# Kernel tuning notes

Hardware: AMD Instinct MI355X
Metric: run time of the kernel (lower is better)

## Reference

```python
import jax, jax.numpy as jnp
import numpy as np

B, V, DIM = 64, 64, 512
H = 2 * DIM  # 1024 hidden units


def setup_inputs() -> dict:
    key = jax.random.key(0)
    ks = jax.random.split(key, 7)
    scale = 0.05
    return {
        "state": jax.random.normal(ks[0], (B, DIM), jnp.float32),
        "action": jax.random.normal(ks[1], (B, DIM), jnp.float32),
        "embed": jax.random.normal(ks[2], (V, DIM), jnp.float32),
        "W1": jax.random.normal(ks[3], (3 * DIM, H), jnp.float32) * scale,
        "b1": jax.random.normal(ks[4], (H,), jnp.float32) * scale,
        "W2": jax.random.normal(ks[5], (H, 1), jnp.float32) * scale,
        "b2": jax.random.normal(ks[6], (1,), jnp.float32) * scale,
    }


def reference(state, action, embed, W1, b1, W2, b2):
    # Original torch code concatenates [cause, effect, ctx] along the feature
    # dim then applies Linear(3*dim, 2*dim). Equivalently, split W1 into three
    # [dim, 2*dim] blocks and sum the three small matmuls (avoids materializing
    # the [B,V,V,3*dim] concat tensor).
    Wc, We, Wx = W1[:DIM], W1[DIM:2 * DIM], W1[2 * DIM:]
    cause_h = embed @ Wc                   # [V, H]
    effect_h = embed @ We                  # [V, H]
    ctx_h = (state + action) @ Wx          # [B, H]
    # broadcast-sum -> [B, V, V, H]
    h = ctx_h[:, None, None, :] + cause_h[None, :, None, :] + effect_h[None, None, :, :] + b1
    h = jax.nn.gelu(h, approximate=False)  # torch nn.GELU default is exact erf
    logits = jnp.einsum("bijh,ho->bij", h, W2) + b2[0]  # [B, V, V]
    scores = jax.nn.sigmoid(logits).mean(axis=0)        # [V, V]
    return scores
```

## Files before the change

kernel.cpp:

```cpp
#include <hip/hip_runtime.h>

#define DIM 512
#define HH  1024
#define NB  64
#define NV  64


static __device__ __forceinline__ float fast_gelu(float x) {
    const float C1 = -0.0713548162f * 1.4426950408889634f;
    const float C0 = -1.5957691216f * 1.4426950408889634f;
    float x2 = x * x;
    float u  = x * fmaf(C1, x2, C0);
    float e  = __builtin_amdgcn_exp2f(u);
    return x * __builtin_amdgcn_rcpf(1.0f + e);
}

extern "C" __global__ __launch_bounds__(256)
void cgl_prep(const float* __restrict__ state, const float* __restrict__ action,
              const float* __restrict__ embed, const float* __restrict__ W1,
              const float* __restrict__ b1, float* __restrict__ ws)
{
    __shared__ float arow[4][64];
    const int m   = blockIdx.x >> 7;
    const int rg  = (blockIdx.x >> 3) & 15;
    const int kc  = blockIdx.x & 7;
    const int tid = threadIdx.x;

    {
        int r = tid >> 6, kk = tid & 63;
        int row = rg * 4 + r, k = kc * 64 + kk;
        arow[r][kk] = (m == 2) ? (state[row * DIM + k] + action[row * DIM + k])
                               : embed[row * DIM + k];
    }
    __syncthreads();

    const float* Wm = W1 + m * DIM * HH + kc * 64 * HH;
    const int c = tid * 4;
    float4 acc0 = {0,0,0,0}, acc1 = {0,0,0,0}, acc2 = {0,0,0,0}, acc3 = {0,0,0,0};
    #pragma unroll 4
    for (int kk = 0; kk < 64; ++kk) {
        const float4 w = *reinterpret_cast<const float4*>(Wm + kk * HH + c);
        float a0 = arow[0][kk], a1 = arow[1][kk], a2 = arow[2][kk], a3 = arow[3][kk];
        acc0.x = fmaf(a0, w.x, acc0.x); acc0.y = fmaf(a0, w.y, acc0.y);
        acc0.z = fmaf(a0, w.z, acc0.z); acc0.w = fmaf(a0, w.w, acc0.w);
        acc1.x = fmaf(a1, w.x, acc1.x); acc1.y = fmaf(a1, w.y, acc1.y);
        acc1.z = fmaf(a1, w.z, acc1.z); acc1.w = fmaf(a1, w.w, acc1.w);
        acc2.x = fmaf(a2, w.x, acc2.x); acc2.y = fmaf(a2, w.y, acc2.y);
        acc2.z = fmaf(a2, w.z, acc2.z); acc2.w = fmaf(a2, w.w, acc2.w);
        acc3.x = fmaf(a3, w.x, acc3.x); acc3.y = fmaf(a3, w.y, acc3.y);
        acc3.z = fmaf(a3, w.z, acc3.z); acc3.w = fmaf(a3, w.w, acc3.w);
    }

    float* ctx   = ws;
    float* cause = ws + NB * HH;
    float* effT  = ws + 2 * NB * HH;
    float4 accs[4] = {acc0, acc1, acc2, acc3};

    if (m == 2 && kc == 0) {
        const float4 bv = *reinterpret_cast<const float4*>(b1 + c);
        #pragma unroll
        for (int r = 0; r < 4; ++r) {
            accs[r].x += bv.x; accs[r].y += bv.y;
            accs[r].z += bv.z; accs[r].w += bv.w;
        }
    }

    #pragma unroll
    for (int r = 0; r < 4; ++r) {
        const int row = rg * 4 + r;
        if (m == 1) {
            atomicAdd(&effT[(c + 0) * NV + row], accs[r].x);
            atomicAdd(&effT[(c + 1) * NV + row], accs[r].y);
            atomicAdd(&effT[(c + 2) * NV + row], accs[r].z);
            atomicAdd(&effT[(c + 3) * NV + row], accs[r].w);
        } else {
            float* base = ((m == 0) ? cause : ctx) + row * HH + c;
            atomicAdd(base + 0, accs[r].x);
            atomicAdd(base + 1, accs[r].y);
            atomicAdd(base + 2, accs[r].z);
            atomicAdd(base + 3, accs[r].w);
        }
    }
}

extern "C" __global__ __launch_bounds__(512, 8)
void cgl_score(const float* __restrict__ ws, const float* __restrict__ W2,
               const float* __restrict__ b2, float* __restrict__ out)
{
    __shared__ float pre[4][HH];
    __shared__ float eff[2][32][64];
    __shared__ float w2s[HH];
    __shared__ float red[8][64];

    const float* ctx   = ws;
    const float* cause = ws + NB * HH;
    const float* effT  = ws + 2 * NB * HH;

    const int i    = blockIdx.x & 63;
    const int bg   = blockIdx.x >> 6;
    const int tid  = threadIdx.x;
    const int wave = tid >> 6;
    const int lane = tid & 63;
    const int bq   = wave & 3;
    const int hh   = wave >> 2;

    for (int idx = tid; idx < 4 * HH; idx += 512) {
        int w = idx >> 10, h = idx & (HH - 1);
        pre[w][h] = ctx[(bg * 4 + w) * HH + h] + cause[i * HH + h];
    }
    for (int h = tid; h < HH; h += 512) w2s[h] = W2[h];

    float acc = 0.0f;
    const int base_h = hh * 512;
    for (int c = 0; c < 16; ++c) {
        __syncthreads();
        for (int idx = tid; idx < 1024; idx += 512) {
            int q = idx >> 9, r = idx & 511;
            reinterpret_cast<float4*>(&eff[q][0][0])[r] =
                reinterpret_cast<const float4*>(effT + (q * 512 + c * 32) * NV)[r];
        }
        __syncthreads();
        #pragma unroll
        for (int dh = 0; dh < 32; ++dh) {
            const int h = base_h + c * 32 + dh;
            float x = pre[bq][h] + eff[hh][dh][lane];
            acc = fmaf(fast_gelu(x), w2s[h], acc);
        }
    }

    red[wave][lane] = acc;
    __syncthreads();
    if (wave < 4) {
        float logit = red[wave][lane] + red[wave + 4][lane] + b2[0];
        float s = __builtin_amdgcn_rcpf(
            1.0f + __builtin_amdgcn_exp2f(-1.4426950408889634f * logit));
        atomicAdd(&out[i * 64 + lane], s * (1.0f / 64.0f));
    }
}

extern "C" void kernel_launch(void* const* d_in, const int* in_sizes, int n_in,
                              void* d_out, int out_size, void* d_ws, size_t ws_size,
                              hipStream_t stream) {
    const float* state  = (const float*)d_in[0];
    const float* action = (const float*)d_in[1];
    const float* embed  = (const float*)d_in[2];
    const float* W1     = (const float*)d_in[3];
    const float* b1     = (const float*)d_in[4];
    const float* W2     = (const float*)d_in[5];
    const float* b2     = (const float*)d_in[6];
    float* ws = (float*)d_ws;

    hipMemsetAsync(d_out, 0, out_size * sizeof(float), stream);
    hipMemsetAsync(d_ws, 0, 3 * NB * HH * sizeof(float), stream);
    cgl_prep<<<384, 256, 0, stream>>>(state, action, embed, W1, b1, ws);
    cgl_score<<<64 * 16, 512, 0, stream>>>(ws, W2, b2, (float*)d_out);
}
```

Before: 201.7 us.

## Replace GELU evaluation with LDS lookup table plus linear interpolation

Adds a small kernel that tabulates GELU(x) minus ReLU(x) on [-8, 8] at a spacing of 1/32, and the scoring kernel copies this table into shared memory. The inner loop then computes relu(x)*w plus an interpolated table correction in place of the exp2/rcp tanh-style GELU. The cause term is now folded into the per-chunk effect staging rather than the precomputed pre array. This swaps transcendental ALU work for LDS gathers with data-dependent indices, which can bank-conflict, and adds interpolation error plus an extra kernel launch.

```diff
diff --git a/kernel.cpp b/kernel.cpp
--- a/kernel.cpp
+++ b/kernel.cpp
@@ -1,18 +1,24 @@
 #include <hip/hip_runtime.h>
+#include <math.h>
 
 #define DIM 512
 #define HH  1024
 #define NB  64
 #define NV  64
+#define TBL_N 513
 
 
-static __device__ __forceinline__ float fast_gelu(float x) {
-    const float C1 = -0.0713548162f * 1.4426950408889634f;
-    const float C0 = -1.5957691216f * 1.4426950408889634f;
-    float x2 = x * x;
-    float u  = x * fmaf(C1, x2, C0);
-    float e  = __builtin_amdgcn_exp2f(u);
-    return x * __builtin_amdgcn_rcpf(1.0f + e);
+extern "C" __global__ void cgl_table(float* __restrict__ tblp)
+{
+    int k = blockIdx.x * 64 + threadIdx.x;
+    if (k < TBL_N) {
+        float x0 = -8.0f + (float)k       * (1.0f / 32.0f);
+        float x1 = -8.0f + (float)(k + 1) * (1.0f / 32.0f);
+        float g0 = 0.5f * x0 * (1.0f + erff(x0 * 0.7071067811865476f));
+        float g1 = 0.5f * x1 * (1.0f + erff(x1 * 0.7071067811865476f));
+        tblp[2 * k + 0] = g0 - fmaxf(x0, 0.0f);
+        tblp[2 * k + 1] = g1 - fmaxf(x1, 0.0f);
+    }
 }
 
 extern "C" __global__ __launch_bounds__(256)
@@ -87,44 +93,63 @@
 void cgl_score(const float* __restrict__ ws, const float* __restrict__ W2,
                const float* __restrict__ b2, float* __restrict__ out)
 {
-    __shared__ float pre[4][HH];
-    __shared__ float eff[2][32][64];
+    __shared__ float comb[2][32][64];
+    __shared__ float ctx_s[4][HH];
     __shared__ float w2s[HH];
+    __shared__ float2 tblp[TBL_N];
     __shared__ float red[8][64];
 
     const float* ctx   = ws;
     const float* cause = ws + NB * HH;
     const float* effT  = ws + 2 * NB * HH;
+    const float* tbg   = ws + 3 * NB * HH;
 
     const int i    = blockIdx.x & 63;
     const int bg   = blockIdx.x >> 6;
     const int tid  = threadIdx.x;
+    const int lane = tid & 63;
     const int wave = tid >> 6;
-    const int lane = tid & 63;
     const int bq   = wave & 3;
     const int hh   = wave >> 2;
 
     for (int idx = tid; idx < 4 * HH; idx += 512) {
         int w = idx >> 10, h = idx & (HH - 1);
-        pre[w][h] = ctx[(bg * 4 + w) * HH + h] + cause[i * HH + h];
+        ctx_s[w][h] = ctx[(bg * 4 + w) * HH + h];
     }
     for (int h = tid; h < HH; h += 512) w2s[h] = W2[h];
+    for (int k = tid; k < TBL_N; k += 512)
+        tblp[k] = make_float2(tbg[2 * k], tbg[2 * k + 1]);
 
     float acc = 0.0f;
-    const int base_h = hh * 512;
     for (int c = 0; c < 16; ++c) {
         __syncthreads();
         for (int idx = tid; idx < 1024; idx += 512) {
-            int q = idx >> 9, r = idx & 511;
-            reinterpret_cast<float4*>(&eff[q][0][0])[r] =
-                reinterpret_cast<const float4*>(effT + (q * 512 + c * 32) * NV)[r];
+            int q  = idx >> 9;
+            int r  = idx & 511;
+            int dh = r >> 4;
+            int jv = r & 15;
+            int h  = q * 512 + c * 32 + dh;
+            float  cs = cause[i * HH + h];
+            float4 e4 = reinterpret_cast<const float4*>(effT + h * NV)[jv];
+            float4 o;
+            o.x = cs + e4.x; o.y = cs + e4.y; o.z = cs + e4.z; o.w = cs + e4.w;
+            reinterpret_cast<float4*>(&comb[q][dh][0])[jv] = o;
         }
         __syncthreads();
         #pragma unroll
         for (int dh = 0; dh < 32; ++dh) {
-            const int h = base_h + c * 32 + dh;
-            float x = pre[bq][h] + eff[hh][dh][lane];
-            acc = fmaf(fast_gelu(x), w2s[h], acc);
+            const int h = hh * 512 + c * 32 + dh;
+            float x  = ctx_s[bq][h] + comb[hh][dh][lane];
+            float xm = fmaxf(x, 0.0f);
+            float u  = fmaf(x, 32.0f, 256.0f);
+            u = fminf(fmaxf(u, 0.0f), 511.0f);
+            int   k = (int)u;
+            float f = u - (float)k;
+            float2 g = tblp[k];
+            float r  = fmaf(f, g.y - g.x, g.x);
+            float w  = w2s[h];
+            acc = fmaf(xm, w, acc);
+            acc = fmaf(r,  w, acc);
         }
     }
 
@@ -144,14 +169,15 @@
     const float* state  = (const float*)d_in[0];
     const float* action = (const float*)d_in[1];
     const float* embed  = (const float*)d_in[2];
+    const float* b1     = (const float*)d_in[4];
     const float* W1     = (const float*)d_in[3];
-    const float* b1     = (const float*)d_in[4];
     const float* W2     = (const float*)d_in[5];
     const float* b2     = (const float*)d_in[6];
     float* ws = (float*)d_ws;
 
     hipMemsetAsync(d_out, 0, out_size * sizeof(float), stream);
     hipMemsetAsync(d_ws, 0, 3 * NB * HH * sizeof(float), stream);
+    cgl_table<<<9, 64, 0, stream>>>(ws + 3 * NB * HH);
     cgl_prep<<<384, 256, 0, stream>>>(state, action, embed, W1, b1, ws);
     cgl_score<<<64 * 16, 512, 0, stream>>>(ws, W2, b2, (float*)d_out);
 }
```

New measurement: 210.4 us. 4.3% more time.

## Pack effect projections as float4 quads and use packed-FP32 math in GELU loop

Applied to the files above, without the earlier changes.

The effect projection buffer moves from an h-major transposed layout to a quad layout that puts four consecutive hidden units per row together. The score kernel can then read float4s from LDS for eff, pre and W2, and it computes the polynomial part of the GELU with v_pk_add/mul/fma_f32 on pairs of values. Four independent accumulators shorten the FMA dependency chain. The goal is fewer LDS instructions and VALU issue slots in the hot loop, at the cost of more registers and inline asm that the compiler cannot schedule around.

```diff
diff --git a/kernel.cpp b/kernel.cpp
--- a/kernel.cpp
+++ b/kernel.cpp
@@ -5,15 +5,19 @@
 #define NB  64
 #define NV  64
 
+typedef float v2f __attribute__((ext_vector_type(2)));
+typedef float v4f __attribute__((ext_vector_type(4)));
 
-static __device__ __forceinline__ float fast_gelu(float x) {
-    const float C1 = -0.0713548162f * 1.4426950408889634f;
-    const float C0 = -1.5957691216f * 1.4426950408889634f;
-    float x2 = x * x;
-    float u  = x * fmaf(C1, x2, C0);
-    float e  = __builtin_amdgcn_exp2f(u);
-    return x * __builtin_amdgcn_rcpf(1.0f + e);
+static __device__ __forceinline__ v2f pk_add(v2f a, v2f b) {
+    v2f d; asm("v_pk_add_f32 %0, %1, %2" : "=v"(d) : "v"(a), "v"(b)); return d;
 }
+static __device__ __forceinline__ v2f pk_mul(v2f a, v2f b) {
+    v2f d; asm("v_pk_mul_f32 %0, %1, %2" : "=v"(d) : "v"(a), "v"(b)); return d;
+}
+static __device__ __forceinline__ v2f pk_fma(v2f a, v2f b, v2f c) {
+    v2f d; asm("v_pk_fma_f32 %0, %1, %2, %3" : "=v"(d) : "v"(a), "v"(b), "v"(c)); return d;
+}
+
 
 extern "C" __global__ __launch_bounds__(256)
 void cgl_prep(const float* __restrict__ state, const float* __restrict__ action,
@@ -53,7 +57,7 @@
 
     float* ctx   = ws;
     float* cause = ws + NB * HH;
-    float* effT  = ws + 2 * NB * HH;
+    float* effQ  = ws + 2 * NB * HH;
     float4 accs[4] = {acc0, acc1, acc2, acc3};
 
     if (m == 2 && kc == 0) {
@@ -69,10 +73,11 @@
     for (int r = 0; r < 4; ++r) {
         const int row = rg * 4 + r;
         if (m == 1) {
-            atomicAdd(&effT[(c + 0) * NV + row], accs[r].x);
-            atomicAdd(&effT[(c + 1) * NV + row], accs[r].y);
-            atomicAdd(&effT[(c + 2) * NV + row], accs[r].z);
-            atomicAdd(&effT[(c + 3) * NV + row], accs[r].w);
+            float* base = effQ + (tid * 64 + row) * 4;
+            atomicAdd(base + 0, accs[r].x);
+            atomicAdd(base + 1, accs[r].y);
+            atomicAdd(base + 2, accs[r].z);
+            atomicAdd(base + 3, accs[r].w);
         } else {
             float* base = ((m == 0) ? cause : ctx) + row * HH + c;
             atomicAdd(base + 0, accs[r].x);
@@ -87,48 +92,79 @@
 void cgl_score(const float* __restrict__ ws, const float* __restrict__ W2,
                const float* __restrict__ b2, float* __restrict__ out)
 {
-    __shared__ float pre[4][HH];
-    __shared__ float eff[2][32][64];
-    __shared__ float w2s[HH];
+    __shared__ v4f pre4[4][256];
+    __shared__ v4f eff4[2][8][64];
+    __shared__ v4f w24[256];
     __shared__ float red[8][64];
 
-    const float* ctx   = ws;
-    const float* cause = ws + NB * HH;
-    const float* effT  = ws + 2 * NB * HH;
+    const v4f* ctx4g   = (const v4f*)ws;
+    const v4f* cause4g = (const v4f*)(ws + NB * HH);
+    const v4f* effQ4g  = (const v4f*)(ws + 2 * NB * HH);
+    const v4f* W24g    = (const v4f*)W2;
 
     const int i    = blockIdx.x & 63;
     const int bg   = blockIdx.x >> 6;
     const int tid  = threadIdx.x;
+    const int lane = tid & 63;
     const int wave = tid >> 6;
-    const int lane = tid & 63;
     const int bq   = wave & 3;
     const int hh   = wave >> 2;
 
-    for (int idx = tid; idx < 4 * HH; idx += 512) {
-        int w = idx >> 10, h = idx & (HH - 1);
-        pre[w][h] = ctx[(bg * 4 + w) * HH + h] + cause[i * HH + h];
+    for (int idx = tid; idx < 1024; idx += 512) {
+        int w = idx >> 8, h4 = idx & 255;
+        v4f c4 = ctx4g[(bg * 4 + w) * 256 + h4];
+        v4f a4 = cause4g[i * 256 + h4];
+        pre4[w][h4] = c4 + a4;
     }
-    for (int h = tid; h < HH; h += 512) w2s[h] = W2[h];
+    for (int h4 = tid; h4 < 256; h4 += 512) w24[h4] = W24g[h4];
 
-    float acc = 0.0f;
-    const int base_h = hh * 512;
+    const float C1 = -0.0713548162f * 1.4426950408889634f;
+    const float C0 = -1.5957691216f * 1.4426950408889634f;
+    const v2f C1p = {C1, C1};
+    const v2f C0p = {C0, C0};
+
+    float accA = 0.0f, accB = 0.0f, accC = 0.0f, accD = 0.0f;
     for (int c = 0; c < 16; ++c) {
         __syncthreads();
-        for (int idx = tid; idx < 1024; idx += 512) {
-            int q = idx >> 9, r = idx & 511;
-            reinterpret_cast<float4*>(&eff[q][0][0])[r] =
-                reinterpret_cast<const float4*>(effT + (q * 512 + c * 32) * NV)[r];
+        for (int t = tid; t < 1024; t += 512) {
+            int q = t >> 9, rem = t & 511, dq = rem >> 6, j = rem & 63;
+            eff4[q][dq][j] = effQ4g[(q * 128 + c * 8 + dq) * 64 + j];
         }
         __syncthreads();
+        const int hq = hh * 128 + c * 8;
         #pragma unroll
-        for (int dh = 0; dh < 32; ++dh) {
-            const int h = base_h + c * 32 + dh;
-            float x = pre[bq][h] + eff[hh][dh][lane];
-            acc = fmaf(fast_gelu(x), w2s[h], acc);
+        for (int dq = 0; dq < 8; ++dq) {
+            v4f e4 = eff4[hh][dq][lane];
+            v4f p4 = pre4[bq][hq + dq];
+            v4f w4 = w24[hq + dq];
+            v2f e01 = __builtin_shufflevector(e4, e4, 0, 1);
+            v2f e23 = __builtin_shufflevector(e4, e4, 2, 3);
+            v2f p01 = __builtin_shufflevector(p4, p4, 0, 1);
+            v2f p23 = __builtin_shufflevector(p4, p4, 2, 3);
+            v2f x01 = pk_add(p01, e01);
+            v2f x23 = pk_add(p23, e23);
+            v2f s01 = pk_mul(x01, x01);
+            v2f s23 = pk_mul(x23, x23);
+            v2f t01 = pk_fma(s01, C1p, C0p);
+            v2f t23 = pk_fma(s23, C1p, C0p);
+            v2f u01 = pk_mul(x01, t01);
+            v2f u23 = pk_mul(x23, t23);
+            float ea = __builtin_amdgcn_exp2f(u01.x);
+            float eb = __builtin_amdgcn_exp2f(u01.y);
+            float ec = __builtin_amdgcn_exp2f(u23.x);
+            float ed = __builtin_amdgcn_exp2f(u23.y);
+            float ra = __builtin_amdgcn_rcpf(1.0f + ea);
+            float rb = __builtin_amdgcn_rcpf(1.0f + eb);
+            float rc = __builtin_amdgcn_rcpf(1.0f + ec);
+            float rd = __builtin_amdgcn_rcpf(1.0f + ed);
+            accA = fmaf(x01.x * ra, w4.x, accA);
+            accB = fmaf(x01.y * rb, w4.y, accB);
+            accC = fmaf(x23.x * rc, w4.z, accC);
+            accD = fmaf(x23.y * rd, w4.w, accD);
         }
     }
 
-    red[wave][lane] = acc;
+    red[wave][lane] = (accA + accB) + (accC + accD);
     __syncthreads();
     if (wave < 4) {
         float logit = red[wave][lane] + red[wave + 4][lane] + b2[0];
```

Result: no change. 203.6 us (+0.9%).
